# Optimization experiments

Hardware: AMD Instinct MI355X
Metric: run time of the kernel (lower is better)

Reference implementation:

```python
import jax, jax.numpy as jnp
import numpy as np

EPS = 1e-08
SPARSITY = 0.1  # fraction of (node, hyperedge) incidences set to 1


def setup_inputs() -> dict:
    key = jax.random.key(0)
    k_x, k_w, k_h, k_W, k_b = jax.random.split(key, 5)
    B, N, E, Din, Dout = 8, 4096, 2048, 256, 256
    x = jax.random.normal(k_x, (B, N, Din), dtype=jnp.float32)
    edge_weight = jax.random.uniform(k_w, (E,), dtype=jnp.float32)
    H = (jax.random.uniform(k_h, (N, E)) < SPARSITY).astype(jnp.float32)
    # nn.Linear params
    bound = 1.0 / np.sqrt(Din)
    W = jax.random.uniform(k_W, (Dout, Din), minval=-bound, maxval=bound, dtype=jnp.float32)
    b = jax.random.uniform(k_b, (Dout,), minval=-bound, maxval=bound, dtype=jnp.float32)
    return {"x": x, "edge_weight": edge_weight, "H": H, "W": W, "b": b}


def _build_adjacency(H, edge_weight):
    # dv = H @ diag(w) @ 1 = H @ w ; de = H.sum(0)
    dv = H @ edge_weight                      # [N]
    de = H.sum(axis=0)                        # [E]
    dv_is = jnp.power(dv + EPS, -0.5)         # Dv^{-1/2} diagonal
    de_inv = jnp.power(de + EPS, -1.0)        # De^{-1} diagonal
    # A = Dv^{-1/2} H W De^{-1} H^T Dv^{-1/2}; apply diagonals as row/col scales
    Hw = H * (edge_weight * de_inv)[None, :]  # [N, E]
    A = (dv_is[:, None] * (Hw @ H.T)) * dv_is[None, :]  # [N, N]
    return A


def reference(x, edge_weight, H, W, b):
    A = _build_adjacency(H, edge_weight)
    xw = jnp.einsum('bnd,od->bno', x, W) + b  # Linear: [B, N, Dout]
    out = jnp.einsum('ij,bjd->bid', A, xw)    # hypergraph propagation
    return out
```

## Files before the change

kernel.cpp:

```cpp
#include <hip/hip_runtime.h>
#include <hip/hip_bf16.h>

typedef __hip_bfloat16 bf16;
typedef __bf16 bfx8 __attribute__((ext_vector_type(8)));
typedef __bf16 bfx4 __attribute__((ext_vector_type(4)));
typedef float f32x4 __attribute__((ext_vector_type(4)));

typedef __attribute__((address_space(3))) void lds_void_t;
typedef const __attribute__((address_space(1))) void gbl_void_t;

__global__ void prep_kernel(const float* __restrict__ H, const float* __restrict__ w,
                            bf16* __restrict__ HT, bf16* __restrict__ Hb,
                            float* __restrict__ de, float* __restrict__ dvr, int N, int E) {
    __shared__ __align__(8) __bf16 tile[64][68];
    int eb = blockIdx.x * 64, nb = blockIdx.y * 64;
    int tid = threadIdx.x;
    int lane = tid & 63, g = tid >> 6;
    int cq = (lane & 15) * 4;
    int rbase = g + ((lane >> 4) << 2);

#pragma unroll
    for (int m = 0; m < 4; m++) {
        int r = rbase + (m << 4);
        f32x4 v = *(const f32x4*)&H[(size_t)(nb + r) * E + eb + cq];
        bfx4 b4;
#pragma unroll
        for (int t = 0; t < 4; t++) b4[t] = (__bf16)v[t];
        *(bfx4*)&tile[r][cq] = b4;
        if (Hb) *(bfx4*)&Hb[(size_t)(nb + r) * E + eb + cq] = b4;
    }
    __syncthreads();

    int c = lane;
    if (g == 0) {
        float s = 0.f;
#pragma unroll 8
        for (int rr = 0; rr < 64; rr++) s += (float)tile[rr][c];
        atomicAdd(&de[eb + c], s);
    } else if (g == 1) {
        float s = 0.f;
#pragma unroll 8
        for (int cc = 0; cc < 64; cc++) s += (float)tile[c][cc] * w[eb + cc];
        atomicAdd(&dvr[nb + c], s);
    }
#pragma unroll
    for (int k = 0; k < 16; k++) {
        int r = g + (k << 2);
        HT[(size_t)(eb + r) * N + nb + c] = (bf16)tile[c][r];
    }
}

__global__ __launch_bounds__(256) void gemm_k3(
    const float* __restrict__ W, const float* __restrict__ x,
    const float* __restrict__ bias, const float* __restrict__ dvr,
    bf16* __restrict__ xs_t) {
    __shared__ __align__(16) bf16 As[256 * 40];
    __shared__ __align__(16) bf16 Bs[64 * 40];

    const int bx = blockIdx.x, z = blockIdx.y;
    const int tid = threadIdx.x;
    const int wave = tid >> 6, lane = tid & 63;
    const int wr = wave * 64;
    const int lcol = lane & 15, quad = lane >> 4;
    const float* xp = x + (size_t)z * 1048576 + (size_t)bx * 64 * 256;

    f32x4 acc[4][4];
#pragma unroll
    for (int i = 0; i < 4; i++)
#pragma unroll
        for (int j = 0; j < 4; j++) acc[i][j] = (f32x4){0.f, 0.f, 0.f, 0.f};

    for (int k0 = 0; k0 < 256; k0 += 32) {
#pragma unroll
        for (int c = 0; c < 4; c++) {
            int ch = tid + c * 256;
            int r = ch >> 2, kc = (ch & 3) << 3;
            f32x4 p0 = *(const f32x4*)&W[(size_t)r * 256 + k0 + kc];
            f32x4 p1 = *(const f32x4*)&W[(size_t)r * 256 + k0 + kc + 4];
            bfx8 va;
#pragma unroll
            for (int t = 0; t < 4; t++) { va[t] = (__bf16)p0[t]; va[4 + t] = (__bf16)p1[t]; }
            *(bfx8*)&As[r * 40 + kc] = va;
        }
        {
            int r = tid >> 2, kc = (tid & 3) << 3;
            f32x4 q0 = *(const f32x4*)&xp[(size_t)r * 256 + k0 + kc];
            f32x4 q1 = *(const f32x4*)&xp[(size_t)r * 256 + k0 + kc + 4];
            bfx8 vb;
#pragma unroll
            for (int t = 0; t < 4; t++) { vb[t] = (__bf16)q0[t]; vb[4 + t] = (__bf16)q1[t]; }
            *(bfx8*)&Bs[r * 40 + kc] = vb;
        }
        __syncthreads();

        bfx8 af[4], bfr[4];
#pragma unroll
        for (int i = 0; i < 4; i++)
            af[i] = *(const bfx8*)&As[(wr + i * 16 + lcol) * 40 + quad * 8];
#pragma unroll
        for (int j = 0; j < 4; j++)
            bfr[j] = *(const bfx8*)&Bs[(j * 16 + lcol) * 40 + quad * 8];
#pragma unroll
        for (int i = 0; i < 4; i++)
#pragma unroll
            for (int j = 0; j < 4; j++)
                acc[i][j] = __builtin_amdgcn_mfma_f32_16x16x32_bf16(af[i], bfr[j], acc[i][j], 0, 0, 0);
        __syncthreads();
    }

#pragma unroll
    for (int j = 0; j < 4; j++) {
        int n = bx * 64 + j * 16 + lcol;
        float dn = rsqrtf(dvr[n] + 1e-8f);
#pragma unroll
        for (int i = 0; i < 4; i++) {
#pragma unroll
            for (int r = 0; r < 4; r++) {
                int o = wr + i * 16 + quad * 4 + r;
                float v = (acc[i][j][r] + bias[o]) * dn;
                xs_t[(size_t)(z * 256 + o) * 4096 + n] = __float2bfloat16(v);
            }
        }
    }
}

#define STG_A(cb, h, u) do { \
    __builtin_amdgcn_global_load_lds((gbl_void_t*)(ga##h##0 + (size_t)(u) * 64), \
        (lds_void_t*)&SM[(cb) * 16384 + (h) * 8192 + dOff], 16, 0, 0); \
    __builtin_amdgcn_global_load_lds((gbl_void_t*)(ga##h##1 + (size_t)(u) * 64), \
        (lds_void_t*)&SM[(cb) * 16384 + (h) * 8192 + 4096 + dOff], 16, 0, 0); \
} while (0)

#define STG_B(cb, h, u) do { \
    __builtin_amdgcn_global_load_lds((gbl_void_t*)(gb##h##0 + (size_t)(u) * 64), \
        (lds_void_t*)&SM[32768 + (cb) * 16384 + (h) * 8192 + dOff], 16, 0, 0); \
    __builtin_amdgcn_global_load_lds((gbl_void_t*)(gb##h##1 + (size_t)(u) * 64), \
        (lds_void_t*)&SM[32768 + (cb) * 16384 + (h) * 8192 + 4096 + dOff], 16, 0, 0); \
} while (0)

#define LDA_(cb, qi, i, kk) \
    (*(const bfx8*)&SM[(cb) * 16384 + aBase + ((qi) * 64 + (i) * 16) * 64 + ra##kk])
#define LDB_(cb, j, kk) \
    (*(const bfx8*)&SM[32768 + (cb) * 16384 + bjb[j] + ra##kk])

#define PH_MFMA(I0, J0) do { \
    __builtin_amdgcn_s_setprio(1); \
    _Pragma("unroll") \
    for (int i_ = 0; i_ < 4; i_++) { \
        _Pragma("unroll") \
        for (int jj_ = 0; jj_ < 2; jj_++) { \
            acc[(I0) + i_][(J0) + jj_] = __builtin_amdgcn_mfma_f32_16x16x32_bf16( \
                af[i_][0], bf[(J0) + jj_][0], acc[(I0) + i_][(J0) + jj_], 0, 0, 0); \
            acc[(I0) + i_][(J0) + jj_] = __builtin_amdgcn_mfma_f32_16x16x32_bf16( \
                af[i_][1], bf[(J0) + jj_][1], acc[(I0) + i_][(J0) + jj_], 0, 0, 0); \
        } \
    } \
    __builtin_amdgcn_s_setprio(0); \
} while (0)

#define CFENCE asm volatile("" ::: "memory")

#define KTILE(cb, uA, uB) do { \
    _Pragma("unroll") \
    for (int i_ = 0; i_ < 4; i_++) { af[i_][0] = LDA_(cb, 0, i_, 0); af[i_][1] = LDA_(cb, 0, i_, 1); } \
    _Pragma("unroll") \
    for (int j_ = 0; j_ < 2; j_++) { bf[j_][0] = LDB_(cb, j_, 0); bf[j_][1] = LDB_(cb, j_, 1); } \
    STG_A((cb) ^ 1, 0, uA); \
    __builtin_amdgcn_s_barrier(); \
    PH_MFMA(0, 0); \
    CFENCE; \
    _Pragma("unroll") \
    for (int j_ = 0; j_ < 2; j_++) { bf[2 + j_][0] = LDB_(cb, 2 + j_, 0); bf[2 + j_][1] = LDB_(cb, 2 + j_, 1); } \
    STG_A((cb) ^ 1, 1, uA); \
    __builtin_amdgcn_s_barrier(); \
    PH_MFMA(0, 2); \
    __builtin_amdgcn_s_barrier(); \
    _Pragma("unroll") \
    for (int i_ = 0; i_ < 4; i_++) { af[i_][0] = LDA_(cb, 1, i_, 0); af[i_][1] = LDA_(cb, 1, i_, 1); } \
    STG_B(cb, 0, uB); \
    __builtin_amdgcn_s_barrier(); \
    PH_MFMA(4, 2); \
    CFENCE; \
    STG_B(cb, 1, uB); \
    __builtin_amdgcn_s_barrier(); \
    PH_MFMA(4, 0); \
    asm volatile("s_waitcnt vmcnt(4)" ::: "memory"); \
    __builtin_amdgcn_s_barrier(); \
} while (0)

__global__ __launch_bounds__(512, 2) void gemm8ph(
    const bf16* __restrict__ A, const bf16* __restrict__ Bt, int Kst, int kLen,
    bf16* __restrict__ S0, bf16* __restrict__ S1, bf16* __restrict__ S2, bf16* __restrict__ S3,
    int ldc) {
    __shared__ __align__(16) bf16 SM[65536];

    const int nx = gridDim.x, ny = gridDim.y;
    const int nwg = nx * ny * gridDim.z;
    const int lin = (blockIdx.z * ny + blockIdx.y) * nx + blockIdx.x;
    const int cpx = nwg >> 3;
    const int swz = (lin & 7) * cpx + (lin >> 3);
    const int bx = swz % nx;
    const int t1 = swz / nx;
    const int by = t1 % ny;
    const int bz = t1 / ny;
    bf16* Cs = (bz == 0) ? S0 : (bz == 1) ? S1 : (bz == 2) ? S2 : S3;
    const int kBase = bz * kLen;
    const int NT = kLen >> 6;

    const int tid = threadIdx.x;
    const int lane = tid & 63, wave = tid >> 6;
    const int lcol = lane & 15, quad = lane >> 4;
    const int wr = (wave >> 2) * 128, wc = (wave & 3) * 64;
    const int aBase = (wave >> 2) * 8192;
    const int xr = lcol & 7;

    const int rowBase = by * 256, colBase = bx * 256;

    const int ra0 = lcol * 64 + ((quad ^ xr) << 3);
    const int ra1 = lcol * 64 + (((4 + quad) ^ xr) << 3);
    int bjb[4];
#pragma unroll
    for (int j = 0; j < 4; j++) {
        int rg = wc + j * 16;
        bjb[j] = ((rg >> 7) * 8192) + ((rg & 127) * 64);
    }

    const int srow = tid >> 3, slot = tid & 7;
    const int r0 = srow, r1 = srow + 64;
    const int sx0 = (slot ^ (r0 & 7)) << 3;
    const int sx1 = (slot ^ (r1 & 7)) << 3;
    const bf16* ga00 = A + (size_t)(rowBase + r0) * Kst + kBase + sx0;
    const bf16* ga01 = A + (size_t)(rowBase + r1) * Kst + kBase + sx1;
    const bf16* ga10 = A + (size_t)(rowBase + 128 + r0) * Kst + kBase + sx0;
    const bf16* ga11 = A + (size_t)(rowBase + 128 + r1) * Kst + kBase + sx1;
    const bf16* gb00 = Bt + (size_t)(colBase + r0) * Kst + kBase + sx0;
    const bf16* gb01 = Bt + (size_t)(colBase + r1) * Kst + kBase + sx1;
    const bf16* gb10 = Bt + (size_t)(colBase + 128 + r0) * Kst + kBase + sx0;
    const bf16* gb11 = Bt + (size_t)(colBase + 128 + r1) * Kst + kBase + sx1;
    const int dOff = tid * 8;

    f32x4 acc[8][4];
#pragma unroll
    for (int i = 0; i < 8; i++)
#pragma unroll
        for (int j = 0; j < 4; j++) acc[i][j] = (f32x4){0.f, 0.f, 0.f, 0.f};
    bfx8 af[4][2], bf[4][2];

    STG_A(0, 0, 0); STG_A(0, 1, 0); STG_B(0, 0, 0); STG_B(0, 1, 0);
    STG_B(1, 0, 1); STG_B(1, 1, 1);
    asm volatile("s_waitcnt vmcnt(4)" ::: "memory");
    __builtin_amdgcn_s_barrier();

    const int nPairs = NT >> 1;
    for (int it = 0; it < nPairs; ++it) {
        int u1 = 2 * it + 1;
        int u2 = 2 * it + 2; if (u2 > NT - 1) u2 = NT - 1;
        int u3 = 2 * it + 3; if (u3 > NT - 1) u3 = NT - 1;
        KTILE(0, u1, u2);
        KTILE(1, u2, u3);
    }

#pragma unroll
    for (int i = 0; i < 8; i++) {
#pragma unroll
        for (int j = 0; j < 4; j++) {
#pragma unroll
            for (int r = 0; r < 4; r++) {
                int grow = rowBase + wr + i * 16 + quad * 4 + r;
                int gcol = colBase + wc + j * 16 + lcol;
                Cs[(size_t)grow * ldc + gcol] = __float2bfloat16(acc[i][j][r]);
            }
        }
    }
}

#define STG5_A(cb, h, u) do { \
    __builtin_amdgcn_global_load_lds((gbl_void_t*)(ga##h##0 + (size_t)(u) * 64), \
        (lds_void_t*)&SM[(cb) * 16384 + (h) * 8192 + dOff], 16, 0, 0); \
    __builtin_amdgcn_global_load_lds((gbl_void_t*)(ga##h##1 + (size_t)(u) * 64), \
        (lds_void_t*)&SM[(cb) * 16384 + (h) * 8192 + 4096 + dOff], 16, 0, 0); \
} while (0)

#define STG5_B(cb, u) do { \
    __builtin_amdgcn_global_load_lds((gbl_void_t*)(gb0 + (size_t)(u) * 64), \
        (lds_void_t*)&SM[32768 + (cb) * 8192 + dOff], 16, 0, 0); \
    __builtin_amdgcn_global_load_lds((gbl_void_t*)(gb1 + (size_t)(u) * 64), \
        (lds_void_t*)&SM[32768 + (cb) * 8192 + 4096 + dOff], 16, 0, 0); \
} while (0)

#define LDA5(cb, i, kk) \
    (*(const bfx8*)&SM[(cb) * 16384 + (wr + (i) * 16) * 64 + ra##kk])
#define LDB5(cb, j, kk) \
    (*(const bfx8*)&SM[32768 + (cb) * 8192 + (wc + (j) * 16) * 64 + ra##kk])

#define PH5_MFMA(J0) do { \
    __builtin_amdgcn_s_setprio(1); \
    _Pragma("unroll") \
    for (int i_ = 0; i_ < 4; i_++) { \
        _Pragma("unroll") \
        for (int jj_ = 0; jj_ < 2; jj_++) { \
            acc[i_][(J0) + jj_] = __builtin_amdgcn_mfma_f32_16x16x32_bf16( \
                af[i_][0], bf[(J0) + jj_][0], acc[i_][(J0) + jj_], 0, 0, 0); \
            acc[i_][(J0) + jj_] = __builtin_amdgcn_mfma_f32_16x16x32_bf16( \
                af[i_][1], bf[(J0) + jj_][1], acc[i_][(J0) + jj_], 0, 0, 0); \
        } \
    } \
    __builtin_amdgcn_s_setprio(0); \
} while (0)

#define KTILE5(cb, uA, uB) do { \
    _Pragma("unroll") \
    for (int i_ = 0; i_ < 4; i_++) { af[i_][0] = LDA5(cb, i_, 0); af[i_][1] = LDA5(cb, i_, 1); } \
    _Pragma("unroll") \
    for (int j_ = 0; j_ < 4; j_++) { bf[j_][0] = LDB5(cb, j_, 0); bf[j_][1] = LDB5(cb, j_, 1); } \
    STG5_A((cb) ^ 1, 0, uA); \
    STG5_A((cb) ^ 1, 1, uA); \
    __builtin_amdgcn_s_barrier(); \
    PH5_MFMA(0); \
    __builtin_amdgcn_s_barrier(); \
    STG5_B(cb, uB); \
    PH5_MFMA(2); \
    asm volatile("s_waitcnt vmcnt(2)" ::: "memory"); \
    __builtin_amdgcn_s_barrier(); \
} while (0)

template <int MODE>
__global__ __launch_bounds__(512, 2) void gemm_tk(
    const bf16* __restrict__ A, const bf16* __restrict__ Bt, int Kst, int NT,
    bf16* __restrict__ Sout, int ldc,
    const float* __restrict__ dvr, float* __restrict__ outF) {
    __shared__ __align__(16) bf16 SM[49152];

    const int nx = gridDim.x, ny = gridDim.y;
    const int nwg = nx * ny * gridDim.z;
    const int lin = (blockIdx.z * ny + blockIdx.y) * nx + blockIdx.x;
    const int cpx = nwg >> 3;
    const int swz = (lin & 7) * cpx + (lin >> 3);
    const int bx = swz % nx;
    const int t1 = swz / nx;
    const int by = t1 % ny;
    const int bz = t1 / ny;
    const int kBase = bz * (NT << 6);

    const int tid = threadIdx.x;
    const int lane = tid & 63, wave = tid >> 6;
    const int lcol = lane & 15, quad = lane >> 4;
    const int wr = (wave >> 1) * 64;
    const int wc = (wave & 1) * 64;
    const int xr = lcol & 7;

    const int rowBase = by * 256, colBase = bx * 128;

    const int ra0 = lcol * 64 + ((quad ^ xr) << 3);
    const int ra1 = lcol * 64 + (((4 + quad) ^ xr) << 3);

    const int srow = tid >> 3, slot = tid & 7;
    const int r0 = srow, r1 = srow + 64;
    const int sx0 = (slot ^ (r0 & 7)) << 3;
    const int sx1 = (slot ^ (r1 & 7)) << 3;
    const bf16* ga00 = A + (size_t)(rowBase + r0) * Kst + kBase + sx0;
    const bf16* ga01 = A + (size_t)(rowBase + r1) * Kst + kBase + sx1;
    const bf16* ga10 = A + (size_t)(rowBase + 128 + r0) * Kst + kBase + sx0;
    const bf16* ga11 = A + (size_t)(rowBase + 128 + r1) * Kst + kBase + sx1;
    const bf16* gb0  = Bt + (size_t)(colBase + r0) * Kst + kBase + sx0;
    const bf16* gb1  = Bt + (size_t)(colBase + r1) * Kst + kBase + sx1;
    const int dOff = tid * 8;

    f32x4 acc[4][4];
#pragma unroll
    for (int i = 0; i < 4; i++)
#pragma unroll
        for (int j = 0; j < 4; j++) acc[i][j] = (f32x4){0.f, 0.f, 0.f, 0.f};
    bfx8 af[4][2], bf[4][2];

    STG5_A(0, 0, 0); STG5_A(0, 1, 0); STG5_B(0, 0);
    STG5_B(1, 1);
    asm volatile("s_waitcnt vmcnt(2)" ::: "memory");
    __builtin_amdgcn_s_barrier();

    for (int it = 0; it < NT / 2; ++it) {
        int u0 = 2 * it, u1 = 2 * it + 1;
        int a0 = u0 + 1;
        int b0 = u0 + 2; if (b0 > NT - 1) b0 = NT - 1;
        int a1 = u1 + 1; if (a1 > NT - 1) a1 = NT - 1;
        int b1 = u1 + 2; if (b1 > NT - 1) b1 = NT - 1;
        KTILE5(0, a0, b0);
        KTILE5(1, a1, b1);
    }

    if (MODE == 0) {
        bf16* Ps = Sout + (size_t)bz * 4194304;
#pragma unroll
        for (int i = 0; i < 4; i++) {
#pragma unroll
            for (int j = 0; j < 4; j++) {
#pragma unroll
                for (int r = 0; r < 4; r++) {
                    int grow = rowBase + wr + i * 16 + quad * 4 + r;
                    int gcol = colBase + wc + j * 16 + lcol;
                    Ps[(size_t)grow * ldc + gcol] = __float2bfloat16(acc[i][j][r]);
                }
            }
        }
    } else {
#pragma unroll
        for (int i = 0; i < 4; i++) {
#pragma unroll
            for (int r = 0; r < 4; r++) {
                int grow = rowBase + wr + i * 16 + quad * 4 + r;
                float dn = rsqrtf(dvr[grow] + 1e-8f);
#pragma unroll
                for (int j = 0; j < 4; j++) {
                    int gcol = colBase + wc + j * 16 + lcol;
                    outF[(size_t)(gcol >> 8) * 1048576 + (size_t)grow * 256 + (gcol & 255)] =
                        acc[i][j][r] * dn;
                }
            }
        }
    }
}

__global__ void combine2_kernel(const bf16* __restrict__ s0, const bf16* __restrict__ s1,
                                const float* __restrict__ w, const float* __restrict__ de,
                                bf16* __restrict__ tt) {
    size_t i = ((size_t)blockIdx.x * 256 + threadIdx.x) * 8;
    int e = (int)(i & 2047);
    bfx8 a = *(const bfx8*)&s0[i];
    bfx8 b = *(const bfx8*)&s1[i];
    bfx8 v;
#pragma unroll
    for (int t = 0; t < 8; t++) {
        float ws = w[e + t] / (de[e + t] + 1e-8f);
        v[t] = (__bf16)(((float)a[t] + (float)b[t]) * ws);
    }
    *(bfx8*)&tt[i] = v;
}

__global__ void transpose_kernel(const bf16* __restrict__ src, bf16* __restrict__ dst,
                                 int R, int C) {
    __shared__ __bf16 t[64][68];
    int cb = blockIdx.x * 64, rb = blockIdx.y * 64;
    int tid = threadIdx.x;
    int lc = tid & 7, lr = tid >> 3;
#pragma unroll
    for (int p = 0; p < 2; p++) {
        int r = lr + p * 32;
        bfx8 v = *(const bfx8*)&src[(size_t)(rb + r) * C + cb + lc * 8];
#pragma unroll
        for (int q = 0; q < 8; q++) t[r][lc * 8 + q] = v[q];
    }
    __syncthreads();
#pragma unroll
    for (int p = 0; p < 2; p++) {
        int c = lr + p * 32;
        bfx8 v;
#pragma unroll
        for (int q = 0; q < 8; q++) v[q] = t[lc * 8 + q][c];
        *(bfx8*)&dst[(size_t)(cb + c) * R + rb + lc * 8] = v;
    }
}

__global__ void combine_out_kernel(const bf16* __restrict__ sA, const bf16* __restrict__ sB,
                                   const float* __restrict__ dvr, float* __restrict__ out) {
    size_t t8 = ((size_t)blockIdx.x * 256 + threadIdx.x) * 8;
    int n = (int)((t8 >> 8) & 4095);
    size_t si = (size_t)n * 2048 + (size_t)(t8 >> 20) * 256 + (t8 & 255);
    bfx8 a = *(const bfx8*)&sA[si];
    bfx8 bb = *(const bfx8*)&sB[si];
    float d = rsqrtf(dvr[n] + 1e-8f);
    f32x4 v0, v1;
#pragma unroll
    for (int t = 0; t < 4; t++) {
        v0[t] = d * ((float)a[t] + (float)bb[t]);
        v1[t] = d * ((float)a[4 + t] + (float)bb[4 + t]);
    }
    *(f32x4*)&out[t8] = v0;
    *(f32x4*)&out[t8 + 4] = v1;
}

extern "C" void kernel_launch(void* const* d_in, const int* in_sizes, int n_in,
                              void* d_out, int out_size, void* d_ws, size_t ws_size,
                              hipStream_t stream) {
    const float* x    = (const float*)d_in[0];
    const float* ew   = (const float*)d_in[1];
    const float* H    = (const float*)d_in[2];
    const float* W    = (const float*)d_in[3];
    const float* bias = (const float*)d_in[4];

    const int N = 4096, E = 2048;

    char* ws = (char*)d_ws;
    float* de   = (float*)(ws);
    float* dvr  = (float*)(ws + 8192);
    bf16*  HT   = (bf16*)(ws + 65536);
    bf16*  xs_t = (bf16*)(ws + 65536 + 16777216);
    bf16*  t_t  = (bf16*)(ws + 65536 + 33554432);
    bf16*  wsHb = (bf16*)(ws + 65536 + 41943040);
    const bool bigws = ws_size >= 58785792ull + 4096ull;

    bf16* s0 = (bf16*)d_out;
    bf16* s1 = s0 + 4194304;

    (void)hipMemsetAsync(ws, 0, 24576, stream);

    prep_kernel<<<dim3(E / 64, N / 64), 256, 0, stream>>>(
        H, ew, HT, bigws ? wsHb : nullptr, de, dvr, N, E);

    gemm_k3<<<dim3(64, 8), 256, 0, stream>>>(W, x, bias, dvr, xs_t);

    gemm_tk<0><<<dim3(16, 8, 2), 512, 0, stream>>>(
        xs_t, HT, 4096, 32, s0, 2048, nullptr, nullptr);

    combine2_kernel<<<dim3(2048), 256, 0, stream>>>(s0, s1, ew, de, t_t);

    if (bigws) {
        gemm_tk<1><<<dim3(16, 16, 1), 512, 0, stream>>>(
            wsHb, t_t, 2048, 32, nullptr, 0, dvr, (float*)d_out);
    } else {
        bf16* HbP = (bf16*)d_out;
        transpose_kernel<<<dim3(64, 32), 256, 0, stream>>>(HT, HbP, 2048, 4096);
        bf16* k5a = HT;
        bf16* k5b = xs_t;
        gemm8ph<<<dim3(8, 16, 2), 512, 0, stream>>>(HbP, t_t, 2048, 1024, k5a, k5b, k5a, k5a, 2048);
        combine_out_kernel<<<dim3(4096), 256, 0, stream>>>(k5a, k5b, dvr, (float*)d_out);
    }
}
```

Before: 197.9 us.

## Fuse split-K partial combine and edge scaling into final propagation GEMM

Result: slower. 210.3 us (+6.3%).

```diff
diff --git a/kernel.cpp b/kernel.cpp
--- a/kernel.cpp
+++ b/kernel.cpp
@@ -420,6 +420,144 @@
     }
 }
 
+#define KT5F(cb, uN) do { \
+    _Pragma("unroll") \
+    for (int i_ = 0; i_ < 4; i_++) { af[i_][0] = LDA5(cb, i_, 0); af[i_][1] = LDA5(cb, i_, 1); } \
+    _Pragma("unroll") \
+    for (int j_ = 0; j_ < 4; j_++) { bf[j_][0] = LDB5(cb, j_, 0); bf[j_][1] = LDB5(cb, j_, 1); } \
+    STG5_A((cb) ^ 1, 0, uN); \
+    STG5_A((cb) ^ 1, 1, uN); \
+    br00 = *(const bfx8*)&S0b[(size_t)(uN) * 64]; \
+    br01 = *(const bfx8*)&S1b[(size_t)(uN) * 64]; \
+    br10 = *(const bfx8*)&S0c[(size_t)(uN) * 64]; \
+    br11 = *(const bfx8*)&S1c[(size_t)(uN) * 64]; \
+    __builtin_amdgcn_s_barrier(); \
+    PH5_MFMA(0); \
+    __builtin_amdgcn_s_barrier(); \
+    asm volatile("s_waitcnt vmcnt(0)" ::: "memory"); \
+    { \
+        f32x4 w0a = *(const f32x4*)&wscL[(uN) * 64 + sx0]; \
+        f32x4 w0b = *(const f32x4*)&wscL[(uN) * 64 + sx0 + 4]; \
+        f32x4 w1a = *(const f32x4*)&wscL[(uN) * 64 + sx1]; \
+        f32x4 w1b = *(const f32x4*)&wscL[(uN) * 64 + sx1 + 4]; \
+        bfx8 o0, o1; \
+        _Pragma("unroll") \
+        for (int t_ = 0; t_ < 4; t_++) { \
+            o0[t_]     = (__bf16)(((float)br00[t_]     + (float)br01[t_])     * w0a[t_]); \
+            o0[4 + t_] = (__bf16)(((float)br00[4 + t_] + (float)br01[4 + t_]) * w0b[t_]); \
+            o1[t_]     = (__bf16)(((float)br10[t_]     + (float)br11[t_])     * w1a[t_]); \
+            o1[4 + t_] = (__bf16)(((float)br10[4 + t_] + (float)br11[4 + t_]) * w1b[t_]); \
+        } \
+        *(bfx8*)&SM[32768 + ((cb) ^ 1) * 8192 + dOff] = o0; \
+        *(bfx8*)&SM[32768 + ((cb) ^ 1) * 8192 + 4096 + dOff] = o1; \
+    } \
+    PH5_MFMA(2); \
+    asm volatile("s_waitcnt lgkmcnt(0)" ::: "memory"); \
+    __builtin_amdgcn_s_barrier(); \
+} while (0)
+
+__global__ __launch_bounds__(512, 2) void gemm_k5f(
+    const bf16* __restrict__ A, const bf16* __restrict__ S0v, const bf16* __restrict__ S1v,
+    const float* __restrict__ ew, const float* __restrict__ de,
+    const float* __restrict__ dvr, float* __restrict__ outF) {
+    __shared__ __align__(16) bf16 SM[49152];
+    __shared__ __align__(16) float wscL[2048];
+    const int Kst = 2048, NT = 32;
+
+    const int nx = gridDim.x, ny = gridDim.y;
+    const int nwg = nx * ny;
+    const int lin = blockIdx.y * nx + blockIdx.x;
+    const int cpx = nwg >> 3;
+    const int swz = (lin & 7) * cpx + (lin >> 3);
+    const int bx = swz % nx;
+    const int by = swz / nx;
+
+    const int tid = threadIdx.x;
+    const int lane = tid & 63, wave = tid >> 6;
+    const int lcol = lane & 15, quad = lane >> 4;
+    const int wr = (wave >> 1) * 64;
+    const int wc = (wave & 1) * 64;
+    const int xr = lcol & 7;
+
+    const int rowBase = by * 256, colBase = bx * 128;
+
+    const int ra0 = lcol * 64 + ((quad ^ xr) << 3);
+    const int ra1 = lcol * 64 + (((4 + quad) ^ xr) << 3);
+
+    const int srow = tid >> 3, slot = tid & 7;
+    const int r0 = srow, r1 = srow + 64;
+    const int sx0 = (slot ^ (r0 & 7)) << 3;
+    const int sx1 = (slot ^ (r1 & 7)) << 3;
+    const bf16* ga00 = A + (size_t)(rowBase + r0) * Kst + sx0;
+    const bf16* ga01 = A + (size_t)(rowBase + r1) * Kst + sx1;
+    const bf16* ga10 = A + (size_t)(rowBase + 128 + r0) * Kst + sx0;
+    const bf16* ga11 = A + (size_t)(rowBase + 128 + r1) * Kst + sx1;
+    const bf16* S0b = S0v + (size_t)(colBase + r0) * 2048 + sx0;
+    const bf16* S1b = S1v + (size_t)(colBase + r0) * 2048 + sx0;
+    const bf16* S0c = S0v + (size_t)(colBase + r1) * 2048 + sx1;
+    const bf16* S1c = S1v + (size_t)(colBase + r1) * 2048 + sx1;
+    const int dOff = tid * 8;
+
+    f32x4 acc[4][4];
+#pragma unroll
+    for (int i = 0; i < 4; i++)
+#pragma unroll
+        for (int j = 0; j < 4; j++) acc[i][j] = (f32x4){0.f, 0.f, 0.f, 0.f};
+    bfx8 af[4][2], bf[4][2];
+    bfx8 br00, br01, br10, br11;
+
+    STG5_A(0, 0, 0); STG5_A(0, 1, 0);
+    br00 = *(const bfx8*)&S0b[0];
+    br01 = *(const bfx8*)&S1b[0];
+    br10 = *(const bfx8*)&S0c[0];
+    br11 = *(const bfx8*)&S1c[0];
+    {
+        int wi = tid * 4;
+#pragma unroll
+        for (int t = 0; t < 4; t++) wscL[wi + t] = ew[wi + t] / (de[wi + t] + 1e-8f);
+    }
+    __syncthreads();
+    {
+        f32x4 w0a = *(const f32x4*)&wscL[sx0];
+        f32x4 w0b = *(const f32x4*)&wscL[sx0 + 4];
+        f32x4 w1a = *(const f32x4*)&wscL[sx1];
+        f32x4 w1b = *(const f32x4*)&wscL[sx1 + 4];
+        bfx8 o0, o1;
+#pragma unroll
+        for (int t = 0; t < 4; t++) {
+            o0[t]     = (__bf16)(((float)br00[t]     + (float)br01[t])     * w0a[t]);
+            o0[4 + t] = (__bf16)(((float)br00[4 + t] + (float)br01[4 + t]) * w0b[t]);
+            o1[t]     = (__bf16)(((float)br10[t]     + (float)br11[t])     * w1a[t]);
+            o1[4 + t] = (__bf16)(((float)br10[4 + t] + (float)br11[4 + t]) * w1b[t]);
+        }
+        *(bfx8*)&SM[32768 + dOff] = o0;
+        *(bfx8*)&SM[32768 + 4096 + dOff] = o1;
+    }
+    __syncthreads();
+
+    for (int it = 0; it < NT / 2; ++it) {
+        int uA = 2 * it + 1;
+        int uB = 2 * it + 2; if (uB > NT - 1) uB = NT - 1;
+        KT5F(0, uA);
+        KT5F(1, uB);
+    }
+
+#pragma unroll
+    for (int i = 0; i < 4; i++) {
+#pragma unroll
+        for (int r = 0; r < 4; r++) {
+            int grow = rowBase + wr + i * 16 + quad * 4 + r;
+            float dn = rsqrtf(dvr[grow] + 1e-8f);
+#pragma unroll
+            for (int j = 0; j < 4; j++) {
+                int gcol = colBase + wc + j * 16 + lcol;
+                outF[(size_t)(gcol >> 8) * 1048576 + (size_t)grow * 256 + (gcol & 255)] =
+                    acc[i][j][r] * dn;
+            }
+        }
+    }
+}
+
 __global__ void combine2_kernel(const bf16* __restrict__ s0, const bf16* __restrict__ s1,
                                 const float* __restrict__ w, const float* __restrict__ de,
                                 bf16* __restrict__ tt) {
@@ -511,12 +649,11 @@
     gemm_tk<0><<<dim3(16, 8, 2), 512, 0, stream>>>(
         xs_t, HT, 4096, 32, s0, 2048, nullptr, nullptr);
 
-    combine2_kernel<<<dim3(2048), 256, 0, stream>>>(s0, s1, ew, de, t_t);
-
     if (bigws) {
-        gemm_tk<1><<<dim3(16, 16, 1), 512, 0, stream>>>(
-            wsHb, t_t, 2048, 32, nullptr, 0, dvr, (float*)d_out);
+        gemm_k5f<<<dim3(16, 16), 512, 0, stream>>>(
+            wsHb, s0, s1, ew, de, dvr, (float*)d_out);
     } else {
+        combine2_kernel<<<dim3(2048), 256, 0, stream>>>(s0, s1, ew, de, t_t);
         bf16* HbP = (bf16*)d_out;
         transpose_kernel<<<dim3(64, 32), 256, 0, stream>>>(HT, HbP, 2048, 4096);
         bf16* k5a = HT;
```
